# Kernel optimization log

Measured on AMD Instinct MI355X. Metric: run time of the kernel, lower is better.

The kernel has to match this reference:

```python
import jax, jax.numpy as jnp
import numpy as np

ALPHA = 0.2  # LeakyReLU negative slope
NEG_INF = -9e15


def setup_inputs() -> dict:
    key = jax.random.key(0)
    k1, k2, k3, k4 = jax.random.split(key, 4)
    B, N, F_IN, F_OUT = 2, 4096, 128, 64
    h = jax.random.normal(k1, (B, N, F_IN), dtype=jnp.float32)
    adj = jax.random.randint(k2, (N, N), 0, 2, dtype=jnp.int32)
    W = jax.random.normal(k3, (F_IN, F_OUT), dtype=jnp.float32) * (1.414 / np.sqrt(F_IN))
    a = jax.random.normal(k4, (2 * F_OUT, 1), dtype=jnp.float32) * 0.1
    return {"h": h, "adj": adj, "W": W, "a": a}


def reference(h, adj, W, a):
    # h: (B, N, F_in), adj: (N, N), W: (F_in, F_out), a: (2*F_out, 1)
    Wh = jnp.einsum("bnf,fo->bno", h, W)  # (B, N, F_out)
    F_out = W.shape[1]
    a1 = a[:F_out, 0]   # attends to source node i
    a2 = a[F_out:, 0]   # attends to target node j
    # e_ij = leakyrelu(a1.Wh_i + a2.Wh_j)  -- rank-1 decomposition of the
    # original cat([Wh_i, Wh_j]) @ a, identical math without O(N^2*2F) tensor.
    s1 = Wh @ a1  # (B, N)
    s2 = Wh @ a2  # (B, N)
    e = s1[:, :, None] + s2[:, None, :]  # (B, N, N)
    e = jnp.where(e >= 0, e, ALPHA * e)  # LeakyReLU
    scores = jnp.where(adj[None, :, :] > 0, e, NEG_INF)
    attention = jax.nn.softmax(scores, axis=-1)
    # dropout=0 (eval/deterministic baseline)
    h_prime = jnp.einsum("bij,bjo->bio", attention, Wh)  # (B, N, F_out)
    return jax.nn.elu(h_prime)  # concat=True branch
```

## Files before the change

kernel.cpp:

```cpp
#include <hip/hip_runtime.h>
#include <hip/hip_bf16.h>
#include <math.h>

#define NB 2
#define NN 4096
#define FIN 128
#define FOUT 64
#define LALPHA 0.2f

#define WS_S1    0
#define WS_S2    (NB*NN)
#define WS_WHT   (2*NB*NN)
#define WS_ABITS (WS_WHT + NB*FOUT*NN/2)

typedef __attribute__((ext_vector_type(8))) short short8;
typedef __attribute__((ext_vector_type(4))) float f32x4;

static __device__ inline unsigned int pack2bf(float x, float y) {
    float2 f2; f2.x = x; f2.y = y;
    __hip_bfloat162 pp = __float22bfloat162_rn(f2);
    return *reinterpret_cast<unsigned int*>(&pp);
}

__global__ __launch_bounds__(256) void k1_proj(const float* __restrict__ h,
                                               const float* __restrict__ W,
                                               const float* __restrict__ a,
                                               const int* __restrict__ adj,
                                               float* __restrict__ ws) {
    __shared__ float tbuf[4][68];
    int gid  = blockIdx.x * 256 + threadIdx.x;
    int wid  = gid >> 6;
    int lane = threadIdx.x & 63;
    int w    = threadIdx.x >> 6;

    int prow  = 2 * blockIdx.x + (threadIdx.x >> 7);
    int pword = threadIdx.x & 127;
    const int4* psrc = (const int4*)&adj[(size_t)prow * NN + pword * 32];
    int4 pv[8];
#pragma unroll
    for (int k = 0; k < 8; ++k) pv[k] = psrc[k];

    const float* hrow = h + (size_t)wid * FIN;
    float h0 = hrow[lane];
    float h1 = hrow[64 + lane];
    float acc = 0.f;
#pragma unroll
    for (int f = 0; f < 64; ++f) {
        float hf = __shfl(h0, f);
        acc = fmaf(hf, W[f * FOUT + lane], acc);
    }
#pragma unroll
    for (int f = 0; f < 64; ++f) {
        float hf = __shfl(h1, f);
        acc = fmaf(hf, W[(64 + f) * FOUT + lane], acc);
    }
    tbuf[w][lane] = acc;
    float v1 = acc * a[lane];
    float v2 = acc * a[FOUT + lane];
#pragma unroll
    for (int off = 32; off; off >>= 1) {
        v1 += __shfl_xor(v1, off);
        v2 += __shfl_xor(v2, off);
    }
    if (lane == 0) {
        ws[WS_S1 + wid] = v1;
        ws[WS_S2 + wid] = v2;
    }

    unsigned int bits = 0;
#pragma unroll
    for (int k = 0; k < 8; ++k) {
        bits |= (pv[k].x != 0 ? 1u : 0u) << (4 * k);
        bits |= (pv[k].y != 0 ? 1u : 0u) << (4 * k + 1);
        bits |= (pv[k].z != 0 ? 1u : 0u) << (4 * k + 2);
        bits |= (pv[k].w != 0 ? 1u : 0u) << (4 * k + 3);
    }
    ((unsigned int*)(ws + WS_ABITS))[(size_t)prow * 128 + pword] = bits;

    __syncthreads();
    if (threadIdx.x < 64) {
        int f = threadIdx.x;
        int wid0 = blockIdx.x * 4;
        int b  = wid0 >> 12;
        int n0 = wid0 & (NN - 1);
        unsigned short* whT = (unsigned short*)(ws + WS_WHT);
        uint2 pk;
        pk.x = pack2bf(tbuf[0][f], tbuf[1][f]);
        pk.y = pack2bf(tbuf[2][f], tbuf[3][f]);
        *(uint2*)&whT[(size_t)(b * FOUT + f) * NN + n0] = pk;
    }
}

__global__ __launch_bounds__(1024, 4) void k3_attn(const float* __restrict__ ws,
                                                   float* __restrict__ out) {
    __shared__ float red[16][2048];
    __shared__ float lred[16][32];
    const int tid  = threadIdx.x;
    const int w    = tid >> 6;
    const int lane = tid & 63;
    const int col  = lane & 15;
    const int quad = lane >> 4;
    const int rt   = blockIdx.x;
    const int i0   = rt * 16;
    const int jbase = w * 256;

    const float* __restrict__ s1 = ws + WS_S1;
    const float* __restrict__ s2 = ws + WS_S2;
    const unsigned short* __restrict__ whT = (const unsigned short*)(ws + WS_WHT);
    const unsigned int* __restrict__ abits = (const unsigned int*)(ws + WS_ABITS);

    unsigned int mrow[8];
    {
        const int4* mp = (const int4*)&abits[(size_t)(i0 + col) * 128 + w * 8];
        *(int4*)&mrow[0] = mp[0];
        *(int4*)&mrow[4] = mp[1];
    }

    float s1a[2];
#pragma unroll
    for (int b = 0; b < 2; ++b) s1a[b] = s1[b * NN + i0 + col];

    f32x4 acc[2][4];
    float lsum[2] = {0.f, 0.f};
#pragma unroll
    for (int b = 0; b < 2; ++b)
#pragma unroll
        for (int nt = 0; nt < 4; ++nt) acc[b][nt] = (f32x4)0.f;

#pragma unroll
    for (int ks = 0; ks < 8; ++ks) {
        const int j8 = jbase + ks * 32 + quad * 8;
        const unsigned int mb = (mrow[ks] >> (quad * 8)) & 0xffu;
#pragma unroll
        for (int b = 0; b < 2; ++b) {
            float4 s2lo = *(const float4*)&s2[b * NN + j8];
            float4 s2hi = *(const float4*)&s2[b * NN + j8 + 4];
            float sj[8] = {s2lo.x, s2lo.y, s2lo.z, s2lo.w,
                           s2hi.x, s2hi.y, s2hi.z, s2hi.w};
            float p[8];
#pragma unroll
            for (int jj = 0; jj < 8; ++jj) {
                float e = s1a[b] + sj[jj];
                e = fmaxf(e, LALPHA * e);
                float pe = __expf(e);
                p[jj] = ((mb >> jj) & 1u) ? pe : 0.f;
                lsum[b] += p[jj];
            }
            unsigned int pk[4];
#pragma unroll
            for (int q = 0; q < 4; ++q) pk[q] = pack2bf(p[2 * q], p[2 * q + 1]);
            short8 afrag = *(short8*)pk;
#pragma unroll
            for (int nt = 0; nt < 4; ++nt) {
                short8 bfrag = *(const short8*)
                    &whT[(size_t)(b * FOUT + nt * 16 + col) * NN + j8];
                acc[b][nt] = __builtin_amdgcn_mfma_f32_16x16x32_bf16(
                    afrag, bfrag, acc[b][nt], 0, 0, 0);
            }
        }
    }

#pragma unroll
    for (int b = 0; b < 2; ++b) {
        float v = lsum[b];
        v += __shfl_xor(v, 16);
        v += __shfl_xor(v, 32);
        if (quad == 0) lred[w][b * 16 + col] = v;
#pragma unroll
        for (int nt = 0; nt < 4; ++nt)
#pragma unroll
            for (int reg = 0; reg < 4; ++reg)
                red[w][(((b * 4 + nt) * 4 + reg) << 6) + lane] = acc[b][nt][reg];
    }
    __syncthreads();

#pragma unroll
    for (int e = 0; e < 2; ++e) {
        int flat = e * 1024 + tid;
        int f    = flat & 63;
        int r16  = (flat >> 6) & 15;
        int b    = flat >> 10;
        int q2   = r16 >> 2, reg = r16 & 3;
        int c2   = f & 15,   nt  = f >> 4;
        int ln   = q2 * 16 + c2;
        int off  = (((b * 4 + nt) * 4 + reg) << 6) + ln;
        float acv = 0.f, l = 0.f;
#pragma unroll
        for (int ww = 0; ww < 16; ++ww) {
            acv += red[ww][off];
            l   += lred[ww][b * 16 + r16];
        }
        float v = acv / l;
        out[(size_t)(((b * NN) + i0 + r16) << 6) + f] = v > 0.f ? v : (__expf(v) - 1.f);
    }
}

extern "C" void kernel_launch(void* const* d_in, const int* in_sizes, int n_in,
                              void* d_out, int out_size, void* d_ws, size_t ws_size,
                              hipStream_t stream) {
    const float* h   = (const float*)d_in[0];
    const int*   adj = (const int*)d_in[1];
    const float* W   = (const float*)d_in[2];
    const float* a   = (const float*)d_in[3];
    float* ws  = (float*)d_ws;
    float* out = (float*)d_out;

    hipLaunchKernelGGL(k1_proj, dim3(NB * NN / 4), dim3(256), 0, stream, h, W, a, adj, ws);
    hipLaunchKernelGGL(k3_attn, dim3(256), dim3(1024), 0, stream, ws, out);
}
```

Measured before the change: 150.0 us.

## Split attention kernel across batch, use tree reduction and exp2 scaling

The attention kernel now launches one block per (batch, row tile) instead of handling both batches in one block, which halves per-block registers and shared memory and doubles the grid. The cross-wave reduction becomes a log-step tree through a smaller shared buffer, with more barriers. Scores are pre-scaled by log2(e) in the projection kernel so the inner loop can use exp2f. The finer grid is meant to improve occupancy and latency hiding. In exchange, the mask bits are now loaded once per batch block rather than once overall.

```diff
diff --git a/kernel.cpp b/kernel.cpp
--- a/kernel.cpp
+++ b/kernel.cpp
@@ -63,8 +63,8 @@
         v2 += __shfl_xor(v2, off);
     }
     if (lane == 0) {
-        ws[WS_S1 + wid] = v1;
-        ws[WS_S2 + wid] = v2;
+        ws[WS_S1 + wid] = v1 * 1.44269504088896f;
+        ws[WS_S2 + wid] = v2 * 1.44269504088896f;
     }
 
     unsigned int bits = 0;
@@ -91,22 +91,24 @@
     }
 }
 
-__global__ __launch_bounds__(1024, 4) void k3_attn(const float* __restrict__ ws,
+__global__ __launch_bounds__(1024, 8) void k3_attn(const float* __restrict__ ws,
                                                    float* __restrict__ out) {
-    __shared__ float red[16][2048];
-    __shared__ float lred[16][32];
+    __shared__ float red[8][1024];
+    __shared__ float lred[16][16];
     const int tid  = threadIdx.x;
     const int w    = tid >> 6;
     const int lane = tid & 63;
     const int col  = lane & 15;
     const int quad = lane >> 4;
-    const int rt   = blockIdx.x;
+    const int rt   = blockIdx.x & 255;
+    const int b    = blockIdx.x >> 8;
     const int i0   = rt * 16;
     const int jbase = w * 256;
 
-    const float* __restrict__ s1 = ws + WS_S1;
-    const float* __restrict__ s2 = ws + WS_S2;
-    const unsigned short* __restrict__ whT = (const unsigned short*)(ws + WS_WHT);
+    const float* __restrict__ s1 = ws + WS_S1 + b * NN;
+    const float* __restrict__ s2 = ws + WS_S2 + b * NN;
+    const unsigned short* __restrict__ whT =
+        (const unsigned short*)(ws + WS_WHT) + (size_t)b * FOUT * NN;
     const unsigned int* __restrict__ abits = (const unsigned int*)(ws + WS_ABITS);
 
     unsigned int mrow[8];
@@ -116,82 +118,85 @@
         *(int4*)&mrow[4] = mp[1];
     }
 
-    float s1a[2];
-#pragma unroll
-    for (int b = 0; b < 2; ++b) s1a[b] = s1[b * NN + i0 + col];
-
-    f32x4 acc[2][4];
-    float lsum[2] = {0.f, 0.f};
-#pragma unroll
-    for (int b = 0; b < 2; ++b)
-#pragma unroll
-        for (int nt = 0; nt < 4; ++nt) acc[b][nt] = (f32x4)0.f;
+    float s1a = s1[i0 + col];
+    f32x4 acc[4];
+    float lsum = 0.f;
+#pragma unroll
+    for (int nt = 0; nt < 4; ++nt) acc[nt] = (f32x4)0.f;
 
 #pragma unroll
     for (int ks = 0; ks < 8; ++ks) {
         const int j8 = jbase + ks * 32 + quad * 8;
         const unsigned int mb = (mrow[ks] >> (quad * 8)) & 0xffu;
-#pragma unroll
-        for (int b = 0; b < 2; ++b) {
-            float4 s2lo = *(const float4*)&s2[b * NN + j8];
-            float4 s2hi = *(const float4*)&s2[b * NN + j8 + 4];
-            float sj[8] = {s2lo.x, s2lo.y, s2lo.z, s2lo.w,
-                           s2hi.x, s2hi.y, s2hi.z, s2hi.w};
-            float p[8];
-#pragma unroll
-            for (int jj = 0; jj < 8; ++jj) {
-                float e = s1a[b] + sj[jj];
-                e = fmaxf(e, LALPHA * e);
-                float pe = __expf(e);
-                p[jj] = ((mb >> jj) & 1u) ? pe : 0.f;
-                lsum[b] += p[jj];
-            }
-            unsigned int pk[4];
-#pragma unroll
-            for (int q = 0; q < 4; ++q) pk[q] = pack2bf(p[2 * q], p[2 * q + 1]);
-            short8 afrag = *(short8*)pk;
-#pragma unroll
-            for (int nt = 0; nt < 4; ++nt) {
-                short8 bfrag = *(const short8*)
-                    &whT[(size_t)(b * FOUT + nt * 16 + col) * NN + j8];
-                acc[b][nt] = __builtin_amdgcn_mfma_f32_16x16x32_bf16(
-                    afrag, bfrag, acc[b][nt], 0, 0, 0);
-            }
-        }
-    }
-
-#pragma unroll
-    for (int b = 0; b < 2; ++b) {
-        float v = lsum[b];
+        float4 s2lo = *(const float4*)&s2[j8];
+        float4 s2hi = *(const float4*)&s2[j8 + 4];
+        float sj[8] = {s2lo.x, s2lo.y, s2lo.z, s2lo.w,
+                       s2hi.x, s2hi.y, s2hi.z, s2hi.w};
+        float p[8];
+#pragma unroll
+        for (int jj = 0; jj < 8; ++jj) {
+            float e = s1a + sj[jj];
+            e = fmaxf(e, LALPHA * e);
+            float pe = exp2f(e);
+            p[jj] = ((mb >> jj) & 1u) ? pe : 0.f;
+            lsum += p[jj];
+        }
+        unsigned int pk[4];
+#pragma unroll
+        for (int q = 0; q < 4; ++q) pk[q] = pack2bf(p[2 * q], p[2 * q + 1]);
+        short8 afrag = *(short8*)pk;
+#pragma unroll
+        for (int nt = 0; nt < 4; ++nt) {
+            short8 bfrag = *(const short8*)
+                &whT[(size_t)(nt * 16 + col) * NN + j8];
+            acc[nt] = __builtin_amdgcn_mfma_f32_16x16x32_bf16(
+                afrag, bfrag, acc[nt], 0, 0, 0);
+        }
+    }
+
+    {
+        float v = lsum;
         v += __shfl_xor(v, 16);
         v += __shfl_xor(v, 32);
-        if (quad == 0) lred[w][b * 16 + col] = v;
+        if (quad == 0) lred[w][col] = v;
+    }
+#pragma unroll
+    for (int half = 8; half >= 1; half >>= 1) {
+        __syncthreads();
+        if (w >= half && w < 2 * half) {
+#pragma unroll
+            for (int nt = 0; nt < 4; ++nt)
+#pragma unroll
+                for (int reg = 0; reg < 4; ++reg)
+                    red[w - half][((nt * 4 + reg) << 6) + lane] = acc[nt][reg];
+        }
+        __syncthreads();
+        if (w < half) {
+#pragma unroll
+            for (int nt = 0; nt < 4; ++nt)
+#pragma unroll
+                for (int reg = 0; reg < 4; ++reg)
+                    acc[nt][reg] += red[w][((nt * 4 + reg) << 6) + lane];
+        }
+    }
+
+    if (w == 0) {
+        float lv[4];
+#pragma unroll
+        for (int reg = 0; reg < 4; ++reg) {
+            float s = 0.f;
+#pragma unroll
+            for (int ww = 0; ww < 16; ++ww) s += lred[ww][quad * 4 + reg];
+            lv[reg] = s;
+        }
 #pragma unroll
         for (int nt = 0; nt < 4; ++nt)
 #pragma unroll
-            for (int reg = 0; reg < 4; ++reg)
-                red[w][(((b * 4 + nt) * 4 + reg) << 6) + lane] = acc[b][nt][reg];
-    }
-    __syncthreads();
-
-#pragma unroll
-    for (int e = 0; e < 2; ++e) {
-        int flat = e * 1024 + tid;
-        int f    = flat & 63;
-        int r16  = (flat >> 6) & 15;
-        int b    = flat >> 10;
-        int q2   = r16 >> 2, reg = r16 & 3;
-        int c2   = f & 15,   nt  = f >> 4;
-        int ln   = q2 * 16 + c2;
-        int off  = (((b * 4 + nt) * 4 + reg) << 6) + ln;
-        float acv = 0.f, l = 0.f;
-#pragma unroll
-        for (int ww = 0; ww < 16; ++ww) {
-            acv += red[ww][off];
-            l   += lred[ww][b * 16 + r16];
-        }
-        float v = acv / l;
-        out[(size_t)(((b * NN) + i0 + r16) << 6) + f] = v > 0.f ? v : (__expf(v) - 1.f);
+            for (int reg = 0; reg < 4; ++reg) {
+                float v = acc[nt][reg] / lv[reg];
+                v = v > 0.f ? v : (__expf(v) - 1.f);
+                out[((size_t)(b * NN + i0 + quad * 4 + reg) << 6) + nt * 16 + col] = v;
+            }
     }
 }
 
@@ -206,5 +211,5 @@
     float* out = (float*)d_out;
 
     hipLaunchKernelGGL(k1_proj, dim3(NB * NN / 4), dim3(256), 0, stream, h, W, a, adj, ws);
-    hipLaunchKernelGGL(k3_attn, dim3(256), dim3(1024), 0, stream, ws, out);
-}
+    hipLaunchKernelGGL(k3_attn, dim3(2 * 256), dim3(1024), 0, stream, ws, out);
+}
```

Result: no change. 148.6 us (-0.9%).

## Split attention blocks by batch, tile 32 rows, reuse Wh fragments, prescale exp2

Applied to the files above, without the earlier changes.

The attention kernel now gives each block one batch and 32 query rows instead of both batches and 16 rows, so each Wh B-fragment is loaded once and reused for two row groups. The projection kernel writes Wh^T in a tiled layout so each k-slice is contiguous for the fragment loads. It also pre-multiplies s1 and s2 by log2(e) so the kernel can use exp2 directly. The adjacency mask rows are now read twice per block, once per batch, instead of once.

```diff
diff --git a/kernel.cpp b/kernel.cpp
--- a/kernel.cpp
+++ b/kernel.cpp
@@ -12,6 +12,7 @@
 #define WS_S2    (NB*NN)
 #define WS_WHT   (2*NB*NN)
 #define WS_ABITS (WS_WHT + NB*FOUT*NN/2)
+
 
 typedef __attribute__((ext_vector_type(8))) short short8;
 typedef __attribute__((ext_vector_type(4))) float f32x4;
@@ -63,8 +64,8 @@
         v2 += __shfl_xor(v2, off);
     }
     if (lane == 0) {
-        ws[WS_S1 + wid] = v1;
-        ws[WS_S2 + wid] = v2;
+        ws[WS_S1 + wid] = v1 * 1.44269504088896f;
+        ws[WS_S2 + wid] = v2 * 1.44269504088896f;
     }
 
     unsigned int bits = 0;
@@ -87,7 +88,8 @@
         uint2 pk;
         pk.x = pack2bf(tbuf[0][f], tbuf[1][f]);
         pk.y = pack2bf(tbuf[2][f], tbuf[3][f]);
-        *(uint2*)&whT[(size_t)(b * FOUT + f) * NN + n0] = pk;
+        size_t off = ((size_t)(b * 128 + (n0 >> 5)) * 2048) + f * 32 + (n0 & 31);
+        *(uint2*)&whT[off] = pk;
     }
 }
 
@@ -100,77 +102,83 @@
     const int lane = tid & 63;
     const int col  = lane & 15;
     const int quad = lane >> 4;
-    const int rt   = blockIdx.x;
-    const int i0   = rt * 16;
+    const int rt   = blockIdx.x & 127;
+    const int b    = blockIdx.x >> 7;
+    const int i0   = rt * 32;
     const int jbase = w * 256;
 
-    const float* __restrict__ s1 = ws + WS_S1;
-    const float* __restrict__ s2 = ws + WS_S2;
-    const unsigned short* __restrict__ whT = (const unsigned short*)(ws + WS_WHT);
+    const float* __restrict__ s1 = ws + WS_S1 + b * NN;
+    const float* __restrict__ s2 = ws + WS_S2 + b * NN;
+    const unsigned short* __restrict__ whT =
+        (const unsigned short*)(ws + WS_WHT) + (size_t)b * FOUT * NN;
     const unsigned int* __restrict__ abits = (const unsigned int*)(ws + WS_ABITS);
 
-    unsigned int mrow[8];
-    {
-        const int4* mp = (const int4*)&abits[(size_t)(i0 + col) * 128 + w * 8];
-        *(int4*)&mrow[0] = mp[0];
-        *(int4*)&mrow[4] = mp[1];
+    unsigned int mrow[2][8];
+#pragma unroll
+    for (int g = 0; g < 2; ++g) {
+        const int4* mp = (const int4*)&abits[(size_t)(i0 + g * 16 + col) * 128 + w * 8];
+        *(int4*)&mrow[g][0] = mp[0];
+        *(int4*)&mrow[g][4] = mp[1];
     }
 
     float s1a[2];
 #pragma unroll
-    for (int b = 0; b < 2; ++b) s1a[b] = s1[b * NN + i0 + col];
+    for (int g = 0; g < 2; ++g) s1a[g] = s1[i0 + g * 16 + col];
 
     f32x4 acc[2][4];
     float lsum[2] = {0.f, 0.f};
 #pragma unroll
-    for (int b = 0; b < 2; ++b)
-#pragma unroll
-        for (int nt = 0; nt < 4; ++nt) acc[b][nt] = (f32x4)0.f;
+    for (int g = 0; g < 2; ++g)
+#pragma unroll
+        for (int nt = 0; nt < 4; ++nt) acc[g][nt] = (f32x4)0.f;
 
 #pragma unroll
     for (int ks = 0; ks < 8; ++ks) {
         const int j8 = jbase + ks * 32 + quad * 8;
-        const unsigned int mb = (mrow[ks] >> (quad * 8)) & 0xffu;
-#pragma unroll
-        for (int b = 0; b < 2; ++b) {
-            float4 s2lo = *(const float4*)&s2[b * NN + j8];
-            float4 s2hi = *(const float4*)&s2[b * NN + j8 + 4];
-            float sj[8] = {s2lo.x, s2lo.y, s2lo.z, s2lo.w,
-                           s2hi.x, s2hi.y, s2hi.z, s2hi.w};
+        const unsigned short* wb = whT + (size_t)(w * 8 + ks) * 2048;
+        short8 bf[4];
+#pragma unroll
+        for (int nt = 0; nt < 4; ++nt)
+            bf[nt] = *(const short8*)&wb[nt * 512 + col * 32 + quad * 8];
+
+        float4 s2lo = *(const float4*)&s2[j8];
+        float4 s2hi = *(const float4*)&s2[j8 + 4];
+        float sj[8] = {s2lo.x, s2lo.y, s2lo.z, s2lo.w,
+                       s2hi.x, s2hi.y, s2hi.z, s2hi.w};
+#pragma unroll
+        for (int g = 0; g < 2; ++g) {
+            const unsigned int mb = (mrow[g][ks] >> (quad * 8)) & 0xffu;
             float p[8];
 #pragma unroll
             for (int jj = 0; jj < 8; ++jj) {
-                float e = s1a[b] + sj[jj];
+                float e = s1a[g] + sj[jj];
                 e = fmaxf(e, LALPHA * e);
-                float pe = __expf(e);
+                float pe = exp2f(e);
                 p[jj] = ((mb >> jj) & 1u) ? pe : 0.f;
-                lsum[b] += p[jj];
+                lsum[g] += p[jj];
             }
             unsigned int pk[4];
 #pragma unroll
             for (int q = 0; q < 4; ++q) pk[q] = pack2bf(p[2 * q], p[2 * q + 1]);
             short8 afrag = *(short8*)pk;
 #pragma unroll
-            for (int nt = 0; nt < 4; ++nt) {
-                short8 bfrag = *(const short8*)
-                    &whT[(size_t)(b * FOUT + nt * 16 + col) * NN + j8];
-                acc[b][nt] = __builtin_amdgcn_mfma_f32_16x16x32_bf16(
-                    afrag, bfrag, acc[b][nt], 0, 0, 0);
-            }
+            for (int nt = 0; nt < 4; ++nt)
+                acc[g][nt] = __builtin_amdgcn_mfma_f32_16x16x32_bf16(
+                    afrag, bf[nt], acc[g][nt], 0, 0, 0);
         }
     }
 
 #pragma unroll
-    for (int b = 0; b < 2; ++b) {
-        float v = lsum[b];
+    for (int g = 0; g < 2; ++g) {
+        float v = lsum[g];
         v += __shfl_xor(v, 16);
         v += __shfl_xor(v, 32);
-        if (quad == 0) lred[w][b * 16 + col] = v;
+        if (quad == 0) lred[w][g * 16 + col] = v;
 #pragma unroll
         for (int nt = 0; nt < 4; ++nt)
 #pragma unroll
             for (int reg = 0; reg < 4; ++reg)
-                red[w][(((b * 4 + nt) * 4 + reg) << 6) + lane] = acc[b][nt][reg];
+                red[w][g * 1024 + ((nt * 4 + reg) << 6) + lane] = acc[g][nt][reg];
     }
     __syncthreads();
 
@@ -178,20 +186,21 @@
     for (int e = 0; e < 2; ++e) {
         int flat = e * 1024 + tid;
         int f    = flat & 63;
-        int r16  = (flat >> 6) & 15;
-        int b    = flat >> 10;
+        int r32  = flat >> 6;
+        int g    = r32 >> 4;
+        int r16  = r32 & 15;
         int q2   = r16 >> 2, reg = r16 & 3;
         int c2   = f & 15,   nt  = f >> 4;
         int ln   = q2 * 16 + c2;
-        int off  = (((b * 4 + nt) * 4 + reg) << 6) + ln;
+        int off  = g * 1024 + ((nt * 4 + reg) << 6) + ln;
         float acv = 0.f, l = 0.f;
 #pragma unroll
         for (int ww = 0; ww < 16; ++ww) {
             acv += red[ww][off];
-            l   += lred[ww][b * 16 + r16];
+            l   += lred[ww][g * 16 + r16];
         }
         float v = acv / l;
-        out[(size_t)(((b * NN) + i0 + r16) << 6) + f] = v > 0.f ? v : (__expf(v) - 1.f);
+        out[((size_t)(b * NN + i0 + r32) << 6) + f] = v > 0.f ? v : (__expf(v) - 1.f);
     }
 }
 
```

Result: faster. 144.6 us (-3.6%).
